# Performance work log

Hardware: AMD Instinct MI355X
Metric: run time of the kernel (lower is better)

The kernel has to match this reference:

```python
import jax, jax.numpy as jnp
import numpy as np

E, H, I, T = 8, 1024, 2816, 512
E4M3_MAX = 448.0  # torch.finfo(float8_e4m3fn).max


def _quantize_to_fp8(w):
    # per-tensor dynamic scaling, identical to quantize_to_fp8 in the source
    amax = jnp.max(jnp.abs(w))
    scale = jnp.maximum(amax / E4M3_MAX, 1e-12)
    fp8 = (w / scale).astype(jnp.float8_e4m3fn)
    return fp8, scale.reshape(1).astype(jnp.float32)


def setup_inputs() -> dict:
    key = jax.random.key(0)
    k1, k2, k3, k4 = jax.random.split(key, 4)
    x = jax.random.normal(k1, (T, H), jnp.float32)
    expert_idx = jax.random.randint(k2, (T,), 0, E)
    # learned 3D expert params (stored compressed as fp8 + per-tensor scale)
    w_gu = jax.random.normal(k3, (E, 2 * I, H), jnp.float32) * 0.02
    w_d = jax.random.normal(k4, (E, H, I), jnp.float32) * 0.02
    w_gu_fp8, w_gu_scale = _quantize_to_fp8(w_gu)
    w_d_fp8, w_d_scale = _quantize_to_fp8(w_d)
    return {
        "x": x,
        "expert_idx": expert_idx,
        "w_gu_fp8": w_gu_fp8,
        "w_gu_scale": w_gu_scale,
        "w_d_fp8": w_d_fp8,
        "w_d_scale": w_d_scale,
    }


def reference(x, expert_idx, w_gu_fp8, w_gu_scale, w_d_fp8, w_d_scale):
    # materialize(): dequantize fp8 -> high precision (fp8.to(dtype) * scale)
    w_gu = w_gu_fp8.astype(jnp.float32) * w_gu_scale  # [E, 2I, H]
    w_d = w_d_fp8.astype(jnp.float32) * w_d_scale     # [E, H, I]
    # inner experts forward: SwiGLU MLP per expert, top-1 routed tokens
    gu = jnp.einsum('th,efh->tef', x, w_gu)            # [T, E, 2I]
    gate, up = jnp.split(gu, 2, axis=-1)               # [T, E, I] each
    h = jax.nn.silu(gate) * up                          # [T, E, I]
    y = jnp.einsum('tei,ehi->teh', h, w_d)              # [T, E, H]
    out = y[jnp.arange(x.shape[0]), expert_idx]         # [T, H] select routed expert
    return out
```

## Files before the change

kernel.cpp:

```cpp
#include <hip/hip_runtime.h>
#include <hip/hip_bf16.h>
#include <stdint.h>

#define E_ 8
#define H_ 1024
#define I_ 2816
#define T_ 512

typedef __attribute__((ext_vector_type(4))) float f32x4;
typedef __attribute__((ext_vector_type(8))) short short8;

typedef __attribute__((address_space(1))) const unsigned GAS;
typedef __attribute__((address_space(3))) unsigned LAS;

__device__ __forceinline__ void dma16(const void* g, void* l) {
    __builtin_amdgcn_global_load_lds((GAS*)g, (LAS*)l, 16, 0, 0);
}
__device__ __forceinline__ unsigned short f2bf(float f) {
    return __builtin_bit_cast(unsigned short, __float2bfloat16(f));
}
__device__ __forceinline__ uint32_t pack_rne(float lo, float hi) {
    return (uint32_t)f2bf(lo) | ((uint32_t)f2bf(hi) << 16);
}
__device__ __forceinline__ uint32_t pack_trunc(float lo, float hi) {
    return (__builtin_bit_cast(uint32_t, hi) & 0xFFFF0000u) |
           (__builtin_bit_cast(uint32_t, lo) >> 16);
}

#define VM6() asm volatile("s_waitcnt vmcnt(6)" ::: "memory")
#define VM0() asm volatile("s_waitcnt vmcnt(0)" ::: "memory")

__global__ __launch_bounds__(256) void route_cvt(const float* __restrict__ x,
                                                 const int* __restrict__ idx,
                                                 int* __restrict__ counts,
                                                 int* __restrict__ bucket,
                                                 unsigned short* __restrict__ xg) {
    int tid = threadIdx.x;
    if (blockIdx.x == 0) {
        if (tid < E_) counts[tid] = 0;
        for (int i = tid; i < E_ * T_; i += 256) bucket[i] = 0;
        __syncthreads();
#pragma unroll
        for (int k = 0; k < 2; ++k) {
            int t = tid + k * 256;
            int e = idx[t];
            int pos = atomicAdd(counts + e, 1);
            bucket[e * T_ + pos] = t;
        }
    }
    int unit = blockIdx.x * 256 + tid;
    const float* xp = x + (size_t)unit * 8;
    float4 a = *(const float4*)xp, b = *(const float4*)(xp + 4);
    uint4 o = make_uint4(pack_rne(a.x, a.y), pack_rne(a.z, a.w),
                         pack_rne(b.x, b.y), pack_rne(b.z, b.w));
    *(uint4*)(xg + (size_t)unit * 8) = o;
}

__global__ __launch_bounds__(256) void gemm1(const unsigned short* __restrict__ xg,
                                             const float* __restrict__ wgu,
                                             const float* __restrict__ sgu_p,
                                             const int* __restrict__ counts,
                                             const int* __restrict__ bucket,
                                             __hip_bfloat16* __restrict__ hbuf) {
    int e = blockIdx.x >> 1, mt = blockIdx.x & 1;
    int cnt = counts[e];
    if (mt * 64 >= cnt) return;
    int f0 = blockIdx.y * 32;

    __shared__ __align__(16) char smem[72 * 1024 + 256];
    int* tok = (int*)(smem + 72 * 1024);
    int tid = threadIdx.x, w = tid >> 6, lane = tid & 63;
    int r16 = lane & 15, kg = lane >> 4;

    float sgu = sgu_p[0];
    asm volatile("" :: "v"(sgu));

    if (tid < 64) tok[tid] = bucket[e * T_ + mt * 64 + tid];
    __syncthreads();

    const char* xb = (const char*)xg;
    const char* srcA[2]; char* dstA[2];
#pragma unroll
    for (int i = 0; i < 2; ++i) {
        int U = (w * 2 + i) * 64 + lane;
        int row = U >> 3, sl = U & 7;
        srcA[i] = xb + (size_t)tok[row] * 2048 + (size_t)((sl ^ (row & 7)) * 16);
        dstA[i] = smem + (w * 2 + i) * 1024;
    }
    const char* wg_e = (const char*)(wgu + (size_t)e * 2 * (size_t)I_ * H_);
    const char* srcB[4]; char* dstB[4];
#pragma unroll
    for (int i = 0; i < 4; ++i) {
        int U = (w * 4 + i) * 64 + lane;
        int row = U >> 4, sl = U & 15;
        int wr = (row < 32) ? (f0 + row) : (I_ + f0 + row - 32);
        srcB[i] = wg_e + (size_t)wr * 4096 + (size_t)((sl ^ (row & 15)) * 16);
        dstB[i] = smem + 24 * 1024 + (w * 4 + i) * 1024;
    }

#define G1_ISSUE(s, buf)                                                     \
    do {                                                                     \
        _Pragma("unroll")                                                    \
        for (int i = 0; i < 2; ++i) dma16(srcA[i] + (size_t)(s) * 128, dstA[i] + (buf) * 8192);  \
        _Pragma("unroll")                                                    \
        for (int i = 0; i < 4; ++i) dma16(srcB[i] + (size_t)(s) * 256, dstB[i] + (buf) * 16384); \
    } while (0)

    G1_ISSUE(0, 0);
    G1_ISSUE(1, 1);

    f32x4 acc[4];
#pragma unroll
    for (int m = 0; m < 4; ++m) acc[m] = (f32x4){0, 0, 0, 0};

    for (int t = 0; t < 16; ++t) {
        VM6();
        __builtin_amdgcn_s_barrier();
        int tp = (t + 2 < 16) ? t + 2 : 15;
        G1_ISSUE(tp, (t + 2) % 3);
        const char* Ab = smem + (t % 3) * 8192;
        const char* Bb = smem + 24 * 1024 + (t % 3) * 16384;
#pragma unroll
        for (int kk = 0; kk < 2; ++kk) {
            int brow = w * 16 + r16;
            int bo = brow * 256 + kk * 128 + kg * 32;
            int sw = r16 << 4;
            float4 b0 = *(float4*)(Bb + (bo ^ sw));
            float4 b1 = *(float4*)(Bb + ((bo + 16) ^ sw));
            uint4 bu = make_uint4(pack_trunc(b0.x, b0.y), pack_trunc(b0.z, b0.w),
                                  pack_trunc(b1.x, b1.y), pack_trunc(b1.z, b1.w));
            short8 B = __builtin_bit_cast(short8, bu);
#pragma unroll
            for (int m = 0; m < 4; ++m) {
                int ar = m * 16 + r16;
                short8 A = *(short8*)(Ab + ((ar * 128 + kk * 64 + kg * 16) ^ ((ar & 7) << 4)));
                acc[m] = __builtin_amdgcn_mfma_f32_16x16x32_bf16(A, B, acc[m], 0, 0, 0);
            }
        }
    }
    VM0();
    __syncthreads();

    float* ex = (float*)smem;
    if (w >= 2) {
        float* dst = ex + (w - 2) * 1024;
#pragma unroll
        for (int m = 0; m < 4; ++m)
#pragma unroll
            for (int j = 0; j < 4; ++j)
                dst[(m * 16 + kg * 4 + j) * 16 + r16] = acc[m][j] * sgu;
    }
    __syncthreads();
    if (w < 2) {
        const float* src = ex + w * 1024;
#pragma unroll
        for (int m = 0; m < 4; ++m)
#pragma unroll
            for (int j = 0; j < 4; ++j) {
                int tr = m * 16 + kg * 4 + j;
                int pos = mt * 64 + tr;
                if (pos < cnt) {
                    float g = acc[m][j] * sgu;
                    float u = src[tr * 16 + r16];
                    float hv = (g / (1.f + __expf(-g))) * u;
                    hbuf[(size_t)tok[tr] * I_ + f0 + w * 16 + r16] = __float2bfloat16(hv);
                }
            }
    }
}

__global__ __launch_bounds__(256) void gemm2(const __hip_bfloat16* __restrict__ hbuf,
                                             const float* __restrict__ wd,
                                             const float* __restrict__ sd_p,
                                             const int* __restrict__ counts,
                                             const int* __restrict__ bucket,
                                             float* __restrict__ out) {
    int e = blockIdx.x >> 1, mt = blockIdx.x & 1;
    int cnt = counts[e];
    if (mt * 64 >= cnt) return;
    int h0 = blockIdx.y * 16;

    __shared__ __align__(16) char smem[72 * 1024 + 256];
    int* tok = (int*)(smem + 72 * 1024);
    int tid = threadIdx.x, w = tid >> 6, lane = tid & 63;
    int r16 = lane & 15, kg = lane >> 4;

    float sd = sd_p[0];
    asm volatile("" :: "v"(sd));

    if (tid < 64) tok[tid] = bucket[e * T_ + mt * 64 + tid];
    __syncthreads();

    const char* hb = (const char*)hbuf;
    const char* srcA[4]; char* dstA[4];
#pragma unroll
    for (int i = 0; i < 4; ++i) {
        int U = (w * 4 + i) * 64 + lane;
        int row = U >> 4, sl = U & 15;
        srcA[i] = hb + (size_t)tok[row] * (I_ * 2) + (size_t)((sl ^ (row & 15)) * 16);
        dstA[i] = smem + (w * 4 + i) * 1024;
    }
    const char* wd_e = (const char*)(wd + (size_t)e * (size_t)H_ * I_);
    const char* srcB[2]; char* dstB[2];
#pragma unroll
    for (int i = 0; i < 2; ++i) {
        int U = (w * 2 + i) * 64 + lane;
        int row = U >> 5, sl = U & 31;
        srcB[i] = wd_e + (size_t)(h0 + row) * ((size_t)I_ * 4) + (size_t)((sl ^ (row & 15)) * 16);
        dstB[i] = smem + 48 * 1024 + (w * 2 + i) * 1024;
    }

#define G2_ISSUE(s, buf)                                                     \
    do {                                                                     \
        _Pragma("unroll")                                                    \
        for (int i = 0; i < 4; ++i) dma16(srcA[i] + (size_t)(s) * 256, dstA[i] + (buf) * 16384); \
        _Pragma("unroll")                                                    \
        for (int i = 0; i < 2; ++i) dma16(srcB[i] + (size_t)(s) * 512, dstB[i] + (buf) * 8192);  \
    } while (0)

    G2_ISSUE(0, 0);
    G2_ISSUE(1, 1);

    f32x4 acc = (f32x4){0, 0, 0, 0};

    for (int t = 0; t < 22; ++t) {
        VM6();
        __builtin_amdgcn_s_barrier();
        int tp = (t + 2 < 22) ? t + 2 : 21;
        G2_ISSUE(tp, (t + 2) % 3);
        const char* Ab = smem + (t % 3) * 16384;
        const char* Bb = smem + 48 * 1024 + (t % 3) * 8192;
#pragma unroll
        for (int kk = 0; kk < 4; ++kk) {
            int bo = r16 * 512 + kk * 128 + kg * 32;
            int sw = r16 << 4;
            float4 b0 = *(float4*)(Bb + (bo ^ sw));
            float4 b1 = *(float4*)(Bb + ((bo + 16) ^ sw));
            uint4 bu = make_uint4(pack_trunc(b0.x, b0.y), pack_trunc(b0.z, b0.w),
                                  pack_trunc(b1.x, b1.y), pack_trunc(b1.z, b1.w));
            short8 B = __builtin_bit_cast(short8, bu);
            int ar = w * 16 + r16;
            short8 A = *(short8*)(Ab + ((ar * 256 + kk * 64 + kg * 16) ^ ((ar & 15) << 4)));
            acc = __builtin_amdgcn_mfma_f32_16x16x32_bf16(A, B, acc, 0, 0, 0);
        }
    }
    VM0();

#pragma unroll
    for (int j = 0; j < 4; ++j) {
        int tr = w * 16 + kg * 4 + j;
        int pos = mt * 64 + tr;
        if (pos < cnt)
            out[(size_t)tok[tr] * H_ + h0 + r16] = acc[j] * sd;
    }
}

extern "C" void kernel_launch(void* const* d_in, const int* in_sizes, int n_in,
                              void* d_out, int out_size, void* d_ws, size_t ws_size,
                              hipStream_t stream) {
    const float* x    = (const float*)d_in[0];
    const int*   eidx = (const int*)d_in[1];
    const float* wgu  = (const float*)d_in[2];
    const float* sgu  = (const float*)d_in[3];
    const float* wd   = (const float*)d_in[4];
    const float* sd   = (const float*)d_in[5];
    float* out = (float*)d_out;

    char* ws = (char*)d_ws;
    int* counts = (int*)ws;
    int* bucket = (int*)(ws + 1024);
    unsigned short* xg = (unsigned short*)(ws + 32768);
    __hip_bfloat16* hbuf = (__hip_bfloat16*)(ws + 1114112);

    route_cvt<<<256, 256, 0, stream>>>(x, eidx, counts, bucket, xg);
    gemm1<<<dim3(E_ * 2, I_ / 32), 256, 0, stream>>>(xg, wgu, sgu, counts, bucket, hbuf);
    gemm2<<<dim3(E_ * 2, H_ / 16), 256, 0, stream>>>(hbuf, wd, sd, counts, bucket, out);
}
```

Measured before the change: 121.7 us.

## Swap grid axes and remap gemm1 warps to token rows for register-only SwiGLU

```diff
diff --git a/kernel.cpp b/kernel.cpp
--- a/kernel.cpp
+++ b/kernel.cpp
@@ -62,10 +62,10 @@
                                              const int* __restrict__ counts,
                                              const int* __restrict__ bucket,
                                              __hip_bfloat16* __restrict__ hbuf) {
-    int e = blockIdx.x >> 1, mt = blockIdx.x & 1;
+    int e = blockIdx.y >> 1, mt = blockIdx.y & 1;
     int cnt = counts[e];
     if (mt * 64 >= cnt) return;
-    int f0 = blockIdx.y * 32;
+    int f0 = blockIdx.x * 32;
 
     __shared__ __align__(16) char smem[72 * 1024 + 256];
     int* tok = (int*)(smem + 72 * 1024);
@@ -84,17 +84,17 @@
     for (int i = 0; i < 2; ++i) {
         int U = (w * 2 + i) * 64 + lane;
         int row = U >> 3, sl = U & 7;
-        srcA[i] = xb + (size_t)tok[row] * 2048 + (size_t)((sl ^ (row & 7)) * 16);
+        srcA[i] = xb + (size_t)tok[row] * 2048 + ((sl ^ (row & 7)) * 16);
         dstA[i] = smem + (w * 2 + i) * 1024;
     }
-    const char* wg_e = (const char*)(wgu + (size_t)e * 2 * (size_t)I_ * H_);
+    const char* wbase = (const char*)wgu + (size_t)e * 2 * (size_t)I_ * H_ * 4;
     const char* srcB[4]; char* dstB[4];
 #pragma unroll
     for (int i = 0; i < 4; ++i) {
         int U = (w * 4 + i) * 64 + lane;
         int row = U >> 4, sl = U & 15;
         int wr = (row < 32) ? (f0 + row) : (I_ + f0 + row - 32);
-        srcB[i] = wg_e + (size_t)wr * 4096 + (size_t)((sl ^ (row & 15)) * 16);
+        srcB[i] = wbase + (size_t)wr * 4096 + ((sl ^ (row & 15)) * 16);
         dstB[i] = smem + 24 * 1024 + (w * 4 + i) * 1024;
     }
 
@@ -111,7 +111,7 @@
 
     f32x4 acc[4];
 #pragma unroll
-    for (int m = 0; m < 4; ++m) acc[m] = (f32x4){0, 0, 0, 0};
+    for (int n = 0; n < 4; ++n) acc[n] = (f32x4){0, 0, 0, 0};
 
     for (int t = 0; t < 16; ++t) {
         VM6();
@@ -122,51 +122,37 @@
         const char* Bb = smem + 24 * 1024 + (t % 3) * 16384;
 #pragma unroll
         for (int kk = 0; kk < 2; ++kk) {
-            int brow = w * 16 + r16;
-            int bo = brow * 256 + kk * 128 + kg * 32;
-            int sw = r16 << 4;
-            float4 b0 = *(float4*)(Bb + (bo ^ sw));
-            float4 b1 = *(float4*)(Bb + ((bo + 16) ^ sw));
-            uint4 bu = make_uint4(pack_trunc(b0.x, b0.y), pack_trunc(b0.z, b0.w),
-                                  pack_trunc(b1.x, b1.y), pack_trunc(b1.z, b1.w));
-            short8 B = __builtin_bit_cast(short8, bu);
-#pragma unroll
-            for (int m = 0; m < 4; ++m) {
-                int ar = m * 16 + r16;
-                short8 A = *(short8*)(Ab + ((ar * 128 + kk * 64 + kg * 16) ^ ((ar & 7) << 4)));
-                acc[m] = __builtin_amdgcn_mfma_f32_16x16x32_bf16(A, B, acc[m], 0, 0, 0);
+            int arow = w * 16 + r16;
+            short8 Af = *(const short8*)(Ab + arow * 128 + (((kk * 4 + kg) ^ (arow & 7)) * 16));
+#pragma unroll
+            for (int n = 0; n < 4; ++n) {
+                int brow = n * 16 + r16;
+                int slot = kk * 8 + kg * 2;
+                float4 b0 = *(const float4*)(Bb + brow * 256 + ((slot ^ (brow & 15)) * 16));
+                float4 b1 = *(const float4*)(Bb + brow * 256 + (((slot + 1) ^ (brow & 15)) * 16));
+                uint4 bu = make_uint4(pack_trunc(b0.x, b0.y), pack_trunc(b0.z, b0.w),
+                                      pack_trunc(b1.x, b1.y), pack_trunc(b1.z, b1.w));
+                short8 Bf = __builtin_bit_cast(short8, bu);
+                acc[n] = __builtin_amdgcn_mfma_f32_16x16x32_bf16(Af, Bf, acc[n], 0, 0, 0);
             }
         }
     }
     VM0();
-    __syncthreads();
-
-    float* ex = (float*)smem;
-    if (w >= 2) {
-        float* dst = ex + (w - 2) * 1024;
-#pragma unroll
-        for (int m = 0; m < 4; ++m)
-#pragma unroll
-            for (int j = 0; j < 4; ++j)
-                dst[(m * 16 + kg * 4 + j) * 16 + r16] = acc[m][j] * sgu;
-    }
-    __syncthreads();
-    if (w < 2) {
-        const float* src = ex + w * 1024;
-#pragma unroll
-        for (int m = 0; m < 4; ++m)
-#pragma unroll
-            for (int j = 0; j < 4; ++j) {
-                int tr = m * 16 + kg * 4 + j;
-                int pos = mt * 64 + tr;
-                if (pos < cnt) {
-                    float g = acc[m][j] * sgu;
-                    float u = src[tr * 16 + r16];
-                    float hv = (g / (1.f + __expf(-g))) * u;
-                    hbuf[(size_t)tok[tr] * I_ + f0 + w * 16 + r16] = __float2bfloat16(hv);
-                }
+
+#pragma unroll
+    for (int n = 0; n < 2; ++n)
+#pragma unroll
+        for (int j = 0; j < 4; ++j) {
+            int tr = w * 16 + kg * 4 + j;
+            int pos = mt * 64 + tr;
+            if (pos < cnt) {
+                float g = acc[n][j] * sgu;
+                float u = acc[n + 2][j] * sgu;
+                float hv = (g / (1.f + __expf(-g))) * u;
+                hbuf[(size_t)tok[tr] * I_ + f0 + n * 16 + r16] = __float2bfloat16(hv);
             }
-    }
+        }
+#undef G1_ISSUE
 }
 
 __global__ __launch_bounds__(256) void gemm2(const __hip_bfloat16* __restrict__ hbuf,
@@ -175,10 +161,10 @@
                                              const int* __restrict__ counts,
                                              const int* __restrict__ bucket,
                                              float* __restrict__ out) {
-    int e = blockIdx.x >> 1, mt = blockIdx.x & 1;
+    int e = blockIdx.y >> 1, mt = blockIdx.y & 1;
     int cnt = counts[e];
     if (mt * 64 >= cnt) return;
-    int h0 = blockIdx.y * 16;
+    int h0 = blockIdx.x * 16;
 
     __shared__ __align__(16) char smem[72 * 1024 + 256];
     int* tok = (int*)(smem + 72 * 1024);
@@ -253,6 +239,7 @@
         if (pos < cnt)
             out[(size_t)tok[tr] * H_ + h0 + r16] = acc[j] * sd;
     }
+#undef G2_ISSUE
 }
 
 extern "C" void kernel_launch(void* const* d_in, const int* in_sizes, int n_in,
@@ -273,6 +260,6 @@
     __hip_bfloat16* hbuf = (__hip_bfloat16*)(ws + 1114112);
 
     route_cvt<<<256, 256, 0, stream>>>(x, eidx, counts, bucket, xg);
-    gemm1<<<dim3(E_ * 2, I_ / 32), 256, 0, stream>>>(xg, wgu, sgu, counts, bucket, hbuf);
-    gemm2<<<dim3(E_ * 2, H_ / 16), 256, 0, stream>>>(hbuf, wd, sd, counts, bucket, out);
-}
+    gemm1<<<dim3(I_ / 32, E_ * 2), 256, 0, stream>>>(xg, wgu, sgu, counts, bucket, hbuf);
+    gemm2<<<dim3(H_ / 16, E_ * 2), 256, 0, stream>>>(hbuf, wd, sd, counts, bucket, out);
+}
```

After: 115.9 us. 4.8% less time.
